# Optimization experiments

Measured on AMD Instinct MI355X. Metric: run time of the kernel, lower is better.

The kernel has to match this reference:

```python
import jax, jax.numpy as jnp
import numpy as np

D_MODEL = 2048
N_HEADS = 16
KV_HEADS = 4
HEAD_DIM = D_MODEL // N_HEADS  # 128
B, T = 2, 2048


def setup_inputs() -> dict:
    key = jax.random.key(0)
    ks = jax.random.split(key, 8)
    s = 1.0 / np.sqrt(D_MODEL)
    x = jax.random.normal(ks[0], (B, T, D_MODEL), dtype=jnp.float32)
    # Linear weights stored as (in_features, out_features); y = x @ W
    Wq = jax.random.normal(ks[1], (D_MODEL, D_MODEL), dtype=jnp.float32) * s
    Wk = jax.random.normal(ks[2], (D_MODEL, KV_HEADS * HEAD_DIM), dtype=jnp.float32) * s
    Wv = jax.random.normal(ks[3], (D_MODEL, KV_HEADS * HEAD_DIM), dtype=jnp.float32) * s
    Wo = jax.random.normal(ks[4], (D_MODEL, D_MODEL), dtype=jnp.float32) * s
    weight_logits = jnp.ones((KV_HEADS,), dtype=jnp.float32)
    weight_values = jnp.ones((KV_HEADS,), dtype=jnp.float32)
    # additive causal mask (1, 1, T, T): 0 on/below diag, -inf above
    neg_inf = jnp.float32(-1e30)
    causal = jnp.tril(jnp.ones((T, T), dtype=bool))
    attn_mask = jnp.where(causal, jnp.float32(0.0), neg_inf)[None, None]
    return {"x": x, "attn_mask": attn_mask, "Wq": Wq, "Wk": Wk, "Wv": Wv,
            "Wo": Wo, "weight_logits": weight_logits, "weight_values": weight_values}


def reference(x, attn_mask, Wq, Wk, Wv, Wo, weight_logits, weight_values):
    Bx, Tx, _ = x.shape
    H, G, D = N_HEADS, KV_HEADS, HEAD_DIM
    group_size = H // G
    head_to_group = jnp.arange(H) // group_size  # (H,)

    q = (x @ Wq).reshape(Bx, Tx, H, D).transpose(0, 2, 1, 3)  # (B,H,T,D)
    k = (x @ Wk).reshape(Bx, Tx, G, D).transpose(0, 2, 1, 3)  # (B,G,T,D)
    v = (x @ Wv).reshape(Bx, Tx, G, D).transpose(0, 2, 1, 3)  # (B,G,T,D)

    # GQA expansion: gather kv groups per head
    k_g = k[:, head_to_group]  # (B,H,T,D)
    v_g = v[:, head_to_group]  # (B,H,T,D)
    # (use_value_weight=False: weight_values unused)

    logit_scale = weight_logits[head_to_group][None, :, None, None]  # (1,H,1,1)
    inv_sqrt_d = jnp.float32(1.0 / np.sqrt(D))
    logits = jnp.einsum('bhqd,bhkd->bhqk', q, k_g) * inv_sqrt_d * logit_scale
    logits = logits + attn_mask
    attn = jax.nn.softmax(logits, axis=-1)  # dropout p=0 -> identity
    y = jnp.einsum('bhqk,bhkd->bhqd', attn, v_g)
    y = y.transpose(0, 2, 1, 3).reshape(Bx, Tx, H * D)
    return y @ Wo
```

## Files before the change

kernel.cpp:

```cpp
#include <hip/hip_runtime.h>
#include <hip/hip_bf16.h>

#define TT 2048
#define DM 2048
#define NH 16
#define KVH 4
#define HD 128

typedef __attribute__((ext_vector_type(8))) short bs8;
typedef __attribute__((ext_vector_type(4))) float fx4;
typedef __attribute__((ext_vector_type(4))) unsigned short us4;

__device__ inline unsigned short f2b(float f) {
  __hip_bfloat16 h = __float2bfloat16(f);
  return *reinterpret_cast<unsigned short*>(&h);
}

__device__ inline void gld_lds16(const ushort* g, ushort* l) {
  __builtin_amdgcn_global_load_lds(
      (const __attribute__((address_space(1))) void*)g,
      (__attribute__((address_space(3))) void*)l,
      16, 0, 0);
}

__global__ __launch_bounds__(256) void cast_f32_bf16(const float* __restrict__ in,
                                                     ushort* __restrict__ out) {
  int i = blockIdx.x * 256 + threadIdx.x;
  float4 v = ((const float4*)in)[i];
  us4 o = {f2b(v.x), f2b(v.y), f2b(v.z), f2b(v.w)};
  ((us4*)out)[i] = o;
}

__global__ __launch_bounds__(256) void transpose_cast_all(
    const float* __restrict__ Wq, const float* __restrict__ Wk,
    const float* __restrict__ Wv, const float* __restrict__ Wo,
    ushort* __restrict__ Wqkvt, ushort* __restrict__ Wot) {
  __shared__ float t[32][33];
  int tx = threadIdx.x, ty = threadIdx.y;
  int n0 = blockIdx.x * 32, k0 = blockIdx.y * 32;
  if (blockIdx.z == 0) {
    const float* src;
    int srcN, col0;
    if (n0 < 2048) { src = Wq; srcN = 2048; col0 = n0; }
    else if (n0 < 2560) { src = Wk; srcN = 512; col0 = n0 - 2048; }
    else { src = Wv; srcN = 512; col0 = n0 - 2560; }
    for (int jj = 0; jj < 4; ++jj)
      t[ty + jj * 8][tx] = src[(size_t)(k0 + ty + jj * 8) * srcN + col0 + tx];
    __syncthreads();
    for (int jj = 0; jj < 4; ++jj)
      Wqkvt[(size_t)(n0 + ty + jj * 8) * 2048 + k0 + tx] = f2b(t[tx][ty + jj * 8]);
  } else {
    if (n0 >= 2048) return;
    for (int jj = 0; jj < 4; ++jj)
      t[ty + jj * 8][tx] = Wo[(size_t)(k0 + ty + jj * 8) * 2048 + n0 + tx];
    __syncthreads();
    for (int jj = 0; jj < 4; ++jj)
      Wot[(size_t)(n0 + ty + jj * 8) * 2048 + k0 + tx] = f2b(t[tx][ty + jj * 8]);
  }
}

__global__ __launch_bounds__(256) void gemm_qkv(const ushort* __restrict__ A,
                                                const ushort* __restrict__ Bt,
                                                ushort* __restrict__ qo,
                                                ushort* __restrict__ ko,
                                                ushort* __restrict__ vo,
                                                int K) {
  __shared__ alignas(16) ushort As[128 * 64];
  __shared__ alignas(16) ushort Bs[128 * 64];
  const int tid = threadIdx.x;
  const int lane = tid & 63;
  const int wid = tid >> 6;
  const int wm = wid >> 1, wn = wid & 1;
  const int quad = lane >> 4, l16 = lane & 15;
  const int bm = blockIdx.y * 128, bn = blockIdx.x * 128;

  fx4 acc[4][4];
  for (int i = 0; i < 4; ++i)
    for (int j = 0; j < 4; ++j) acc[i][j] = (fx4){0.f, 0.f, 0.f, 0.f};

  const int r8 = lane >> 3, s8 = lane & 7;
  for (int k0 = 0; k0 < K; k0 += 64) {
    for (int i = 0; i < 4; ++i) {
      int m = i * 32 + wid * 8 + r8;
      int c = s8 ^ (m & 7);
      gld_lds16(A + (size_t)(bm + m) * K + k0 + c * 8, As + (i * 32 + wid * 8) * 64);
      gld_lds16(Bt + (size_t)(bn + m) * K + k0 + c * 8, Bs + (i * 32 + wid * 8) * 64);
    }
    __syncthreads();
    for (int ks = 0; ks < 2; ++ks) {
      bs8 af[4], bf[4];
      for (int mt = 0; mt < 4; ++mt) {
        int m = wm * 64 + mt * 16 + l16;
        int c = ks * 4 + quad;
        int slot = c ^ (m & 7);
        af[mt] = *(const bs8*)(As + m * 64 + slot * 8);
      }
      for (int nt = 0; nt < 4; ++nt) {
        int n = wn * 64 + nt * 16 + l16;
        int c = ks * 4 + quad;
        int slot = c ^ (n & 7);
        bf[nt] = *(const bs8*)(Bs + n * 64 + slot * 8);
      }
      for (int mt = 0; mt < 4; ++mt)
        for (int nt = 0; nt < 4; ++nt)
          acc[mt][nt] = __builtin_amdgcn_mfma_f32_16x16x32_bf16(af[mt], bf[nt],
                                                                acc[mt][nt], 0, 0, 0);
    }
    __syncthreads();
  }

  for (int mt = 0; mt < 4; ++mt)
    for (int nt = 0; nt < 4; ++nt)
      for (int r = 0; r < 4; ++r) {
        int row = bm + wm * 64 + mt * 16 + quad * 4 + r;
        int col = bn + wn * 64 + nt * 16 + l16;
        float v = acc[mt][nt][r];
        if (bn < 2048) {
          qo[(size_t)row * 2048 + col] = f2b(v);
        } else if (bn < 2560) {
          int kc = col - 2048;
          int b = row >> 11, t = row & 2047;
          int gg = kc >> 7, d = kc & 127;
          ko[((size_t)(b * KVH + gg) * TT + t) * HD + d] = f2b(v);
        } else {
          int vc = col - 2560;
          int b = row >> 11, t = row & 2047;
          int gg = vc >> 7, d = vc & 127;
          vo[((size_t)(b * KVH + gg) * HD + d) * TT + t] = f2b(v);
        }
      }
}

__global__ __launch_bounds__(256) void gemm_out(const ushort* __restrict__ A,
                                                const ushort* __restrict__ Bt,
                                                float* __restrict__ Cout,
                                                int N, int K) {
  __shared__ alignas(16) ushort As[128 * 64];
  __shared__ alignas(16) ushort Bs[128 * 64];
  const int tid = threadIdx.x;
  const int lane = tid & 63;
  const int wid = tid >> 6;
  const int wm = wid >> 1, wn = wid & 1;
  const int quad = lane >> 4, l16 = lane & 15;
  const int bm = blockIdx.y * 128, bn = blockIdx.x * 128;

  fx4 acc[4][4];
  for (int i = 0; i < 4; ++i)
    for (int j = 0; j < 4; ++j) acc[i][j] = (fx4){0.f, 0.f, 0.f, 0.f};

  const int r8 = lane >> 3, s8 = lane & 7;
  for (int k0 = 0; k0 < K; k0 += 64) {
    for (int i = 0; i < 4; ++i) {
      int m = i * 32 + wid * 8 + r8;
      int c = s8 ^ (m & 7);
      gld_lds16(A + (size_t)(bm + m) * K + k0 + c * 8, As + (i * 32 + wid * 8) * 64);
      gld_lds16(Bt + (size_t)(bn + m) * K + k0 + c * 8, Bs + (i * 32 + wid * 8) * 64);
    }
    __syncthreads();
    for (int ks = 0; ks < 2; ++ks) {
      bs8 af[4], bf[4];
      for (int mt = 0; mt < 4; ++mt) {
        int m = wm * 64 + mt * 16 + l16;
        int c = ks * 4 + quad;
        int slot = c ^ (m & 7);
        af[mt] = *(const bs8*)(As + m * 64 + slot * 8);
      }
      for (int nt = 0; nt < 4; ++nt) {
        int n = wn * 64 + nt * 16 + l16;
        int c = ks * 4 + quad;
        int slot = c ^ (n & 7);
        bf[nt] = *(const bs8*)(Bs + n * 64 + slot * 8);
      }
      for (int mt = 0; mt < 4; ++mt)
        for (int nt = 0; nt < 4; ++nt)
          acc[mt][nt] = __builtin_amdgcn_mfma_f32_16x16x32_bf16(af[mt], bf[nt],
                                                                acc[mt][nt], 0, 0, 0);
    }
    __syncthreads();
  }

  for (int mt = 0; mt < 4; ++mt)
    for (int nt = 0; nt < 4; ++nt)
      for (int r = 0; r < 4; ++r) {
        int row = bm + wm * 64 + mt * 16 + quad * 4 + r;
        int col = bn + wn * 64 + nt * 16 + l16;
        Cout[(size_t)row * N + col] = acc[mt][nt][r];
      }
}

__global__ __launch_bounds__(512, 4) void attn_kernel(const ushort* __restrict__ qb,
                                                      const ushort* __restrict__ kb,
                                                      const ushort* __restrict__ vt,
                                                      ushort* __restrict__ yb,
                                                      const float* __restrict__ wlog) {
  __shared__ alignas(16) ushort Ks[64 * 128];
  __shared__ alignas(16) ushort Vs[128 * 64];
  __shared__ alignas(16) ushort Ps[128 * 72];

  const int bid = blockIdx.x;
  const int qt = (bid & 256) ? (bid & 15) : 15 - (bid & 15);
  const int h = (bid >> 4) & 15;
  const int b = bid >> 8;
  const int g = h >> 2;
  const int tid = threadIdx.x;
  const int lane = tid & 63;
  const int wid = tid >> 6;
  const int quad = lane >> 4;
  const int l16 = lane & 15;
  const int qw = qt * 128 + wid * 16;

  const float scale = wlog[g] * 0.08838834764831845f;

  bs8 qf[4];
  {
    int q = qw + l16;
    const ushort* qrow = qb + ((size_t)(b * TT + q)) * DM + h * HD;
#pragma unroll
    for (int ks = 0; ks < 4; ++ks)
      qf[ks] = *(const bs8*)(qrow + ks * 32 + quad * 8);
  }

  float m_i = -INFINITY;
  float l_i = 0.f;
  fx4 o[8];
#pragma unroll
  for (int i = 0; i < 8; ++i) o[i] = (fx4){0.f, 0.f, 0.f, 0.f};

  const ushort* kbase = kb + (size_t)(b * KVH + g) * TT * HD;
  const ushort* vbase = vt + (size_t)(b * KVH + g) * HD * TT;

  const ushort* kp;
  const ushort* vp;
  {
    int keyr = wid * 4 + (lane >> 4);
    int si = lane & 15;
    int ck = (si & 8) | ((si ^ keyr) & 7);
    kp = kbase + (size_t)keyr * HD + ck * 8;
    int dr = wid * 8 + (lane >> 3);
    int s8 = lane & 7;
    int cv = s8 ^ (dr & 7);
    vp = vbase + (size_t)dr * TT + cv * 8;
  }

  const int jmax = 2 * qt + 1;
  for (int j = 0; j <= jmax; ++j) {
    gld_lds16(kp, Ks + wid * 512);
    gld_lds16(kp + 32 * HD, Ks + 4096 + wid * 512);
    gld_lds16(vp, Vs + wid * 512);
    gld_lds16(vp + 64 * TT, Vs + 4096 + wid * 512);
    kp += 64 * HD;
    vp += 64;
    __syncthreads();

    if (j * 64 <= qw + 15) {
      fx4 s[4];
#pragma unroll
      for (int mt = 0; mt < 4; ++mt) s[mt] = (fx4){0.f, 0.f, 0.f, 0.f};
#pragma unroll
      for (int mt = 0; mt < 4; ++mt) {
        bs8 a[4];
        int key = mt * 16 + l16;
#pragma unroll
        for (int ks = 0; ks < 4; ++ks) {
          int c = ks * 4 + quad;
          int slot = (c & 8) | ((c ^ key) & 7);
          a[ks] = *(const bs8*)(Ks + key * 128 + slot * 8);
        }
#pragma unroll
        for (int ks = 0; ks < 4; ++ks)
          s[mt] = __builtin_amdgcn_mfma_f32_16x16x32_bf16(a[ks], qf[ks],
                                                          s[mt], 0, 0, 0);
      }

      const int q = qw + l16;
      if (j * 64 + 63 > qw) {
#pragma unroll
        for (int mt = 0; mt < 4; ++mt)
#pragma unroll
          for (int r = 0; r < 4; ++r) {
            int key = j * 64 + mt * 16 + quad * 4 + r;
            if (key > q) s[mt][r] = -1e30f;
          }
      }
      float mx = s[0][0];
#pragma unroll
      for (int mt = 0; mt < 4; ++mt)
#pragma unroll
        for (int r = 0; r < 4; ++r) mx = fmaxf(mx, s[mt][r]);
      mx = fmaxf(mx, __shfl_xor(mx, 16));
      mx = fmaxf(mx, __shfl_xor(mx, 32));
      float m_new = fmaxf(m_i, mx);
      float alpha = __expf((m_i - m_new) * scale);
      float negb = -m_new * scale;
      float sum = 0.f;
#pragma unroll
      for (int mt = 0; mt < 4; ++mt)
#pragma unroll
        for (int r = 0; r < 4; ++r) {
          float pv = __expf(fmaf(s[mt][r], scale, negb));
          s[mt][r] = pv;
          sum += pv;
        }
      sum += __shfl_xor(sum, 16);
      sum += __shfl_xor(sum, 32);
      l_i = l_i * alpha + sum;
      m_i = m_new;
#pragma unroll
      for (int dmt = 0; dmt < 8; ++dmt)
#pragma unroll
        for (int r = 0; r < 4; ++r) o[dmt][r] *= alpha;

      int qrow = wid * 16 + l16;
#pragma unroll
      for (int mt = 0; mt < 4; ++mt) {
        us4 pw = {f2b(s[mt][0]), f2b(s[mt][1]), f2b(s[mt][2]), f2b(s[mt][3])};
        *(us4*)(Ps + qrow * 72 + mt * 16 + quad * 4) = pw;
      }

#pragma unroll
      for (int ks = 0; ks < 2; ++ks) {
        bs8 pb = *(const bs8*)(Ps + qrow * 72 + ks * 32 + quad * 8);
#pragma unroll
        for (int dmt = 0; dmt < 8; ++dmt) {
          int d = dmt * 16 + l16;
          int c = ks * 4 + quad;
          int slot = c ^ (d & 7);
          bs8 va = *(const bs8*)(Vs + d * 64 + slot * 8);
          o[dmt] = __builtin_amdgcn_mfma_f32_16x16x32_bf16(va, pb, o[dmt], 0, 0, 0);
        }
      }
    }
    __syncthreads();
  }

  {
    float inv = 1.0f / l_i;
    int q = qw + l16;
    ushort* yrow = yb + ((size_t)(b * TT + q)) * DM + h * HD;
#pragma unroll
    for (int dmt = 0; dmt < 8; ++dmt) {
      us4 w = {f2b(o[dmt][0] * inv), f2b(o[dmt][1] * inv),
               f2b(o[dmt][2] * inv), f2b(o[dmt][3] * inv)};
      *(us4*)(yrow + dmt * 16 + quad * 4) = w;
    }
  }
}

extern "C" void kernel_launch(void* const* d_in, const int* in_sizes, int n_in,
                              void* d_out, int out_size, void* d_ws, size_t ws_size,
                              hipStream_t stream) {
  const float* x = (const float*)d_in[0];
  const float* Wq = (const float*)d_in[2];
  const float* Wk = (const float*)d_in[3];
  const float* Wv = (const float*)d_in[4];
  const float* Wo = (const float*)d_in[5];
  const float* wlog = (const float*)d_in[6];

  char* ws = (char*)d_ws;
  ushort* xb = (ushort*)ws;     ws += (size_t)4096 * 2048 * 2;
  ushort* Wqkvt = (ushort*)ws;  ws += (size_t)3072 * 2048 * 2;
  ushort* Wot = (ushort*)ws;    ws += (size_t)2048 * 2048 * 2;
  ushort* qbuf = (ushort*)ws;   ws += (size_t)4096 * 2048 * 2;
  ushort* kbuf = (ushort*)ws;   ws += (size_t)2 * KVH * 2048 * 128 * 2;
  ushort* vbuf = (ushort*)ws;   ws += (size_t)2 * KVH * 2048 * 128 * 2;
  ushort* ybuf = (ushort*)ws;   ws += (size_t)4096 * 2048 * 2;

  cast_f32_bf16<<<8192, 256, 0, stream>>>(x, xb);
  transpose_cast_all<<<dim3(96, 64, 2), dim3(32, 8), 0, stream>>>(
      Wq, Wk, Wv, Wo, Wqkvt, Wot);
  gemm_qkv<<<dim3(24, 32), 256, 0, stream>>>(xb, Wqkvt, qbuf, kbuf, vbuf, 2048);
  attn_kernel<<<512, 512, 0, stream>>>(qbuf, kbuf, vbuf, ybuf, wlog);
  gemm_out<<<dim3(16, 32), 256, 0, stream>>>(ybuf, Wot, (float*)d_out, 2048, 2048);
}
```

Baseline: 313.9 us.

## Stage GEMM epilogues through LDS for vectorized stores and split V transpose

GEMM epilogues now write accumulators into shared memory, then emit 16-byte vectorized global stores. This replaces scattered 2-byte stores, especially the strided transposed V write, which moves into a separate small transpose kernel. The x cast is folded into the weight prep kernel to save a launch. The output GEMM now rounds results to bf16 before writing fp32, which adds precision loss.

Result: no change. 310.6 us (-1.0%).

```diff
diff --git a/kernel.cpp b/kernel.cpp
--- a/kernel.cpp
+++ b/kernel.cpp
@@ -10,10 +10,16 @@
 typedef __attribute__((ext_vector_type(8))) short bs8;
 typedef __attribute__((ext_vector_type(4))) float fx4;
 typedef __attribute__((ext_vector_type(4))) unsigned short us4;
+typedef __attribute__((ext_vector_type(8))) unsigned short us8;
 
 __device__ inline unsigned short f2b(float f) {
   __hip_bfloat16 h = __float2bfloat16(f);
   return *reinterpret_cast<unsigned short*>(&h);
+}
+
+__device__ inline float b2f(unsigned short u) {
+  unsigned int v = ((unsigned int)u) << 16;
+  return *reinterpret_cast<float*>(&v);
 }
 
 __device__ inline void gld_lds16(const ushort* g, ushort* l) {
@@ -23,20 +29,26 @@
       16, 0, 0);
 }
 
-__global__ __launch_bounds__(256) void cast_f32_bf16(const float* __restrict__ in,
-                                                     ushort* __restrict__ out) {
-  int i = blockIdx.x * 256 + threadIdx.x;
-  float4 v = ((const float4*)in)[i];
-  us4 o = {f2b(v.x), f2b(v.y), f2b(v.z), f2b(v.w)};
-  ((us4*)out)[i] = o;
-}
-
-__global__ __launch_bounds__(256) void transpose_cast_all(
-    const float* __restrict__ Wq, const float* __restrict__ Wk,
-    const float* __restrict__ Wv, const float* __restrict__ Wo,
+__global__ __launch_bounds__(256) void prep_kernel(
+    const float* __restrict__ x, const float* __restrict__ Wq,
+    const float* __restrict__ Wk, const float* __restrict__ Wv,
+    const float* __restrict__ Wo, ushort* __restrict__ xb,
     ushort* __restrict__ Wqkvt, ushort* __restrict__ Wot) {
+  int tx = threadIdx.x, ty = threadIdx.y;
+  if (blockIdx.z == 2) {
+    int lin = (blockIdx.y * 96 + blockIdx.x) * 256 + ty * 32 + tx;
+#pragma unroll
+    for (int it = 0; it < 2; ++it) {
+      int i = lin + it * (6144 * 256);
+      if (i < (TT * 2 * DM) / 4) {
+        float4 v = ((const float4*)x)[i];
+        us4 o = {f2b(v.x), f2b(v.y), f2b(v.z), f2b(v.w)};
+        ((us4*)xb)[i] = o;
+      }
+    }
+    return;
+  }
   __shared__ float t[32][33];
-  int tx = threadIdx.x, ty = threadIdx.y;
   int n0 = blockIdx.x * 32, k0 = blockIdx.y * 32;
   if (blockIdx.z == 0) {
     const float* src;
@@ -59,14 +71,16 @@
   }
 }
 
+#define EPI_STRIDE 136
 __global__ __launch_bounds__(256) void gemm_qkv(const ushort* __restrict__ A,
                                                 const ushort* __restrict__ Bt,
                                                 ushort* __restrict__ qo,
                                                 ushort* __restrict__ ko,
                                                 ushort* __restrict__ vo,
                                                 int K) {
-  __shared__ alignas(16) ushort As[128 * 64];
-  __shared__ alignas(16) ushort Bs[128 * 64];
+  __shared__ alignas(16) ushort smem[128 * EPI_STRIDE];
+  ushort* As = smem;
+  ushort* Bs = smem + 8192;
   const int tid = threadIdx.x;
   const int lane = tid & 63;
   const int wid = tid >> 6;
@@ -112,31 +126,55 @@
   for (int mt = 0; mt < 4; ++mt)
     for (int nt = 0; nt < 4; ++nt)
       for (int r = 0; r < 4; ++r) {
-        int row = bm + wm * 64 + mt * 16 + quad * 4 + r;
-        int col = bn + wn * 64 + nt * 16 + l16;
-        float v = acc[mt][nt][r];
-        if (bn < 2048) {
-          qo[(size_t)row * 2048 + col] = f2b(v);
-        } else if (bn < 2560) {
-          int kc = col - 2048;
-          int b = row >> 11, t = row & 2047;
-          int gg = kc >> 7, d = kc & 127;
-          ko[((size_t)(b * KVH + gg) * TT + t) * HD + d] = f2b(v);
-        } else {
-          int vc = col - 2560;
-          int b = row >> 11, t = row & 2047;
-          int gg = vc >> 7, d = vc & 127;
-          vo[((size_t)(b * KVH + gg) * HD + d) * TT + t] = f2b(v);
-        }
-      }
+        int row = wm * 64 + mt * 16 + quad * 4 + r;
+        int col = wn * 64 + nt * 16 + l16;
+        smem[row * EPI_STRIDE + col] = f2b(acc[mt][nt][r]);
+      }
+  __syncthreads();
+  const int rsel = tid >> 4;
+  const int csel = tid & 15;
+  for (int ii = 0; ii < 8; ++ii) {
+    int row = ii * 16 + rsel;
+    us8 chunk = *(const us8*)(smem + row * EPI_STRIDE + csel * 8);
+    int row_g = bm + row;
+    int colc = bn + csel * 8;
+    if (bn < 2048) {
+      *(us8*)(qo + (size_t)row_g * 2048 + colc) = chunk;
+    } else {
+      int b = row_g >> 11, t = row_g & 2047;
+      if (bn < 2560) {
+        int kc = colc - 2048;
+        int gg = kc >> 7, d = kc & 127;
+        *(us8*)(ko + ((size_t)(b * KVH + gg) * TT + t) * HD + d) = chunk;
+      } else {
+        int vc = colc - 2560;
+        int gg = vc >> 7, d = vc & 127;
+        *(us8*)(vo + ((size_t)(b * KVH + gg) * TT + t) * HD + d) = chunk;
+      }
+    }
+  }
+}
+
+__global__ __launch_bounds__(256) void transpose_v(const ushort* __restrict__ vin,
+                                                   ushort* __restrict__ vout) {
+  __shared__ ushort tl[32][33];
+  int tx = threadIdx.x, ty = threadIdx.y;
+  int t0 = blockIdx.x * 32, d0 = blockIdx.y * 32;
+  size_t base = (size_t)blockIdx.z * TT * HD;
+  for (int jj = 0; jj < 4; ++jj)
+    tl[ty + jj * 8][tx] = vin[base + (size_t)(t0 + ty + jj * 8) * HD + d0 + tx];
+  __syncthreads();
+  for (int jj = 0; jj < 4; ++jj)
+    vout[base + (size_t)(d0 + ty + jj * 8) * TT + t0 + tx] = tl[tx][ty + jj * 8];
 }
 
 __global__ __launch_bounds__(256) void gemm_out(const ushort* __restrict__ A,
                                                 const ushort* __restrict__ Bt,
                                                 float* __restrict__ Cout,
                                                 int N, int K) {
-  __shared__ alignas(16) ushort As[128 * 64];
-  __shared__ alignas(16) ushort Bs[128 * 64];
+  __shared__ alignas(16) ushort smem[128 * EPI_STRIDE];
+  ushort* As = smem;
+  ushort* Bs = smem + 8192;
   const int tid = threadIdx.x;
   const int lane = tid & 63;
   const int wid = tid >> 6;
@@ -182,10 +220,23 @@
   for (int mt = 0; mt < 4; ++mt)
     for (int nt = 0; nt < 4; ++nt)
       for (int r = 0; r < 4; ++r) {
-        int row = bm + wm * 64 + mt * 16 + quad * 4 + r;
-        int col = bn + wn * 64 + nt * 16 + l16;
-        Cout[(size_t)row * N + col] = acc[mt][nt][r];
-      }
+        int row = wm * 64 + mt * 16 + quad * 4 + r;
+        int col = wn * 64 + nt * 16 + l16;
+        smem[row * EPI_STRIDE + col] = f2b(acc[mt][nt][r]);
+      }
+  __syncthreads();
+  const int rsel = tid >> 4;
+  const int csel = tid & 15;
+  for (int ii = 0; ii < 8; ++ii) {
+    int row = ii * 16 + rsel;
+    us8 chunk = *(const us8*)(smem + row * EPI_STRIDE + csel * 8);
+    int row_g = bm + row;
+    int colc = bn + csel * 8;
+    float4 lo = {b2f(chunk[0]), b2f(chunk[1]), b2f(chunk[2]), b2f(chunk[3])};
+    float4 hi = {b2f(chunk[4]), b2f(chunk[5]), b2f(chunk[6]), b2f(chunk[7])};
+    *(float4*)(Cout + (size_t)row_g * N + colc) = lo;
+    *(float4*)(Cout + (size_t)row_g * N + colc + 4) = hi;
+  }
 }
 
 __global__ __launch_bounds__(512, 4) void attn_kernel(const ushort* __restrict__ qb,
@@ -362,13 +413,14 @@
   ushort* Wot = (ushort*)ws;    ws += (size_t)2048 * 2048 * 2;
   ushort* qbuf = (ushort*)ws;   ws += (size_t)4096 * 2048 * 2;
   ushort* kbuf = (ushort*)ws;   ws += (size_t)2 * KVH * 2048 * 128 * 2;
+  ushort* vtmp = (ushort*)ws;   ws += (size_t)2 * KVH * 2048 * 128 * 2;
   ushort* vbuf = (ushort*)ws;   ws += (size_t)2 * KVH * 2048 * 128 * 2;
   ushort* ybuf = (ushort*)ws;   ws += (size_t)4096 * 2048 * 2;
 
-  cast_f32_bf16<<<8192, 256, 0, stream>>>(x, xb);
-  transpose_cast_all<<<dim3(96, 64, 2), dim3(32, 8), 0, stream>>>(
-      Wq, Wk, Wv, Wo, Wqkvt, Wot);
-  gemm_qkv<<<dim3(24, 32), 256, 0, stream>>>(xb, Wqkvt, qbuf, kbuf, vbuf, 2048);
+  prep_kernel<<<dim3(96, 64, 3), dim3(32, 8), 0, stream>>>(
+      x, Wq, Wk, Wv, Wo, xb, Wqkvt, Wot);
+  gemm_qkv<<<dim3(24, 32), 256, 0, stream>>>(xb, Wqkvt, qbuf, kbuf, vtmp, 2048);
+  transpose_v<<<dim3(64, 4, 8), dim3(32, 8), 0, stream>>>(vtmp, vbuf);
   attn_kernel<<<512, 512, 0, stream>>>(qbuf, kbuf, vbuf, ybuf, wlog);
   gemm_out<<<dim3(16, 32), 256, 0, stream>>>(ybuf, Wot, (float*)d_out, 2048, 2048);
 }
```
